# Optimization experiments

Hardware: AMD Instinct MI355X
Metric: run time of the kernel (lower is better)

## Reference

```python
import jax, jax.numpy as jnp
import numpy as np

V = 32          # num_variables
T = 48          # num_time_bins
D = 512         # d_model
H = 8           # num_heads
HD = D // H     # head_dim = 64
OD = 16         # observation_dim
B = 4


def setup_inputs() -> dict:
    key = jax.random.key(0)
    ks = jax.random.split(key, 20)
    s = 0.02
    inp = {
        'h': jax.random.normal(ks[0], (B, T, V, D), jnp.float32),
        'observation_state': jax.random.normal(ks[1], (B, T, V, 2), jnp.float32),
        'Wq': jax.random.normal(ks[2], (D, D), jnp.float32) * s,
        'bq': jnp.zeros((D,), jnp.float32),
        'Wk': jax.random.normal(ks[3], (D, D), jnp.float32) * s,
        'bk': jnp.zeros((D,), jnp.float32),
        'Wv': jax.random.normal(ks[4], (D, D), jnp.float32) * s,
        'bv': jnp.zeros((D,), jnp.float32),
        'Wo': jax.random.normal(ks[5], (D, D), jnp.float32) * s,
        'bo': jnp.zeros((D,), jnp.float32),
        'Woq': jax.random.normal(ks[6], (2, H * OD), jnp.float32) * 0.5,
        'boq': jnp.zeros((H * OD,), jnp.float32),
        'Wok': jax.random.normal(ks[7], (2, H * OD), jnp.float32) * 0.5,
        'bok': jnp.zeros((H * OD,), jnp.float32),
        'variable_bias': jax.random.normal(ks[8], (H, V, V), jnp.float32) * 0.01,
        'relative_time_bias': jax.random.normal(ks[9], (H, 2 * T - 1), jnp.float32) * 0.01,
    }
    return inp


def reference(h, observation_state, Wq, bq, Wk, bk, Wv, bv, Wo, bo,
              Woq, boq, Wok, bok, variable_bias, relative_time_bias):
    N = T * V
    scale = 1.0 / np.sqrt(HD)
    obs_scale = 1.0 / np.sqrt(OD)

    # static index buffers (constants)
    flat_var_ids = jnp.tile(jnp.arange(V), T)                       # [N]
    flat_time_ids = jnp.repeat(jnp.arange(T), V)                    # [N]
    rel_index = flat_time_ids[:, None] - flat_time_ids[None, :] + (T - 1)  # [N,N]

    fh = h.reshape(B, N, D)
    fo = observation_state.reshape(B, N, 2)

    def heads(x, nh, hd):
        return x.reshape(B, N, nh, hd).transpose(0, 2, 1, 3)  # [B,H,N,hd]

    q = heads(fh @ Wq + bq, H, HD)
    k = heads(fh @ Wk + bk, H, HD)
    v = heads(fh @ Wv + bv, H, HD)
    oq = heads(fo @ Woq + boq, H, OD)
    ok = heads(fo @ Wok + bok, H, OD)

    content = jnp.einsum('bhnd,bhmd->bhnm', q, k) * scale
    obs = jnp.einsum('bhnd,bhmd->bhnm', oq, ok) * obs_scale
    var_scores = variable_bias[:, flat_var_ids[:, None], flat_var_ids[None, :]]  # [H,N,N]
    time_scores = relative_time_bias[:, rel_index]                                # [H,N,N]

    scores = content + obs + var_scores[None] + time_scores[None]
    attn = jax.nn.softmax(scores, axis=-1)  # dropout off (inference)
    out = jnp.einsum('bhnm,bhmd->bhnd', attn, v)
    out = out.transpose(0, 2, 1, 3).reshape(B, N, D)
    out = out @ Wo + bo
    return out.reshape(B, T, V, D)
```

## Files before the change

### kernel.cpp

```cpp
#include <hip/hip_runtime.h>
#include <math.h>

typedef __bf16 bf16x8 __attribute__((ext_vector_type(8)));
typedef float f32x4 __attribute__((ext_vector_type(4)));

#define NB 4
#define NT 48
#define NV 32
#define ND 512
#define NH 8
#define NN 1536
#define NBN 6144
#define L2E 1.44269504f

#define GLOAD_LDS(g, l) \
    __builtin_amdgcn_global_load_lds( \
        (const __attribute__((address_space(1))) void*)(g), \
        (__attribute__((address_space(3))) void*)(l), 16, 0, 0)

__global__ __launch_bounds__(256) void prep(
    const float* __restrict__ h, const float* __restrict__ obs,
    const float* __restrict__ Wq, const float* __restrict__ Wk,
    const float* __restrict__ Wv, const float* __restrict__ Wo,
    const float* __restrict__ bq, const float* __restrict__ bk,
    const float* __restrict__ bv,
    const float* __restrict__ Wok, const float* __restrict__ bok,
    __bf16* __restrict__ h_bf, __bf16* __restrict__ WcatT,
    __bf16* __restrict__ WoT, float* __restrict__ biascat,
    __bf16* __restrict__ kx)
{
    __shared__ float ts[64][68];
    const int tid = threadIdx.x;
    const int bx = blockIdx.x;
    if (bx < 1536) {
        int t = bx * 256 + tid;
        const float4* src = (const float4*)h + (size_t)t * 2;
        float4 a = src[0], b = src[1];
        __bf16 r[8] = {(__bf16)a.x, (__bf16)a.y, (__bf16)a.z, (__bf16)a.w,
                       (__bf16)b.x, (__bf16)b.y, (__bf16)b.z, (__bf16)b.w};
        *(uint4*)(h_bf + (size_t)t * 8) = *(uint4*)r;
    } else if (bx < 1792) {
        int bw = bx - 1536;
        const int p = bw >> 6, tile = bw & 63;
        const int k0 = (tile >> 3) * 64, c0 = (tile & 7) * 64;
        const float* W = (p == 0) ? Wq : (p == 1) ? Wk : (p == 2) ? Wv : Wo;
        const float scale = (p == 0) ? 0.125f * L2E : 1.0f;
        #pragma unroll
        for (int i = 0; i < 4; i++) {
            int r = (tid >> 4) + i * 16;
            float4 v = *(const float4*)(W + (size_t)(k0 + r) * 512 + c0 + (tid & 15) * 4);
            *(float4*)&ts[r][(tid & 15) * 4] = v;
        }
        __syncthreads();
        __bf16 tmp[16];
        #pragma unroll
        for (int j = 0; j < 16; j++)
            tmp[j] = (__bf16)(ts[(tid & 3) * 16 + j][tid >> 2] * scale);
        int crow = c0 + (tid >> 2);
        __bf16* dst = (p < 3)
            ? WcatT + ((size_t)(p * 512 + crow)) * 512 + k0 + (tid & 3) * 16
            : WoT   + ((size_t)crow) * 512 + k0 + (tid & 3) * 16;
        *(uint4*)dst = *(uint4*)tmp;
        *(uint4*)(dst + 8) = *(uint4*)(tmp + 8);
        if (p < 3 && k0 == 0 && tid < 64) {
            const float* bb = (p == 0) ? bq : (p == 1) ? bk : bv;
            biascat[p * 512 + c0 + tid] = bb[c0 + tid] * scale;
        }
    } else {
        int t = (bx - 1792) * 256 + tid;
        int row = t >> 1, half = t & 1;
        __bf16* dst = kx + (size_t)row * 96 + 64 + half * 16;
        if (half == 0) {
            int bh = row / NN, n = row - bh * NN;
            int b = bh >> 3, hh = bh & 7;
            size_t bn = (size_t)b * NN + n;
            float o0 = obs[bn * 2], o1 = obs[bn * 2 + 1];
            int f = hh * 16;
            __bf16 tmp[16];
            #pragma unroll
            for (int j = 0; j < 16; j++)
                tmp[j] = (__bf16)(o0 * Wok[f + j] + o1 * Wok[128 + f + j] + bok[f + j]);
            *(uint4*)dst       = *(uint4*)tmp;
            *(uint4*)(dst + 8) = *(uint4*)(tmp + 8);
        } else {
            uint4 z = {0, 0, 0, 0};
            *(uint4*)dst       = z;
            *(uint4*)(dst + 8) = z;
        }
    }
}

template<int TM, bool BF16OUT>
__global__ __launch_bounds__(256) void gemm_mfma(
    const __bf16* __restrict__ A, const __bf16* __restrict__ Bt,
    const float* __restrict__ bias, float* __restrict__ Cf,
    __bf16* __restrict__ qarr, __bf16* __restrict__ kx,
    __bf16* __restrict__ vt)
{
    constexpr int MT = TM / 32;
    __shared__ __align__(16) char smem[34816];
    char* const As0 = smem;
    char* const As1 = smem + TM * 64;
    char* const Bs0 = smem + TM * 128;
    char* const Bs1 = smem + TM * 128 + 8192;
    const int tid = threadIdx.x;
    const int w = tid >> 6, lane = tid & 63;
    const int quad = lane >> 4, l16 = lane & 15;
    const int wm = w >> 1, wn = w & 1;
    const int n0 = blockIdx.x * 128, m0 = blockIdx.y * TM;

    const int sm = tid >> 2;
    const int sk = ((tid & 3) ^ ((sm >> 1) & 3)) * 8;
    const __bf16* aptr = A  + (size_t)(m0 + sm) * 512 + sk;
    const __bf16* bptr = Bt + (size_t)(n0 + sm) * 512 + sk;

    f32x4 zero4 = {0.f, 0.f, 0.f, 0.f};
    f32x4 acc[MT][4];
    #pragma unroll
    for (int i = 0; i < MT; i++)
        #pragma unroll
        for (int j = 0; j < 4; j++) acc[i][j] = zero4;

    auto STAGE = [&](char* dA, char* dB, int kt) {
        GLOAD_LDS(aptr + kt, dA + tid * 16);
        if (TM == 128) GLOAD_LDS(aptr + 64 * 512 + kt, dA + 4096 + tid * 16);
        GLOAD_LDS(bptr + kt, dB + tid * 16);
        GLOAD_LDS(bptr + 64 * 512 + kt, dB + 4096 + tid * 16);
    };
    auto COMPUTE = [&](const char* Asb, const char* Bsb) {
        bf16x8 af[MT], bfr[4];
        #pragma unroll
        for (int mt = 0; mt < MT; mt++) {
            int rr = wm * (TM / 2) + mt * 16 + l16;
            af[mt] = *(const bf16x8*)(Asb + rr * 64 + (quad ^ ((rr >> 1) & 3)) * 16);
        }
        #pragma unroll
        for (int nt = 0; nt < 4; nt++) {
            int rr = wn * 64 + nt * 16 + l16;
            bfr[nt] = *(const bf16x8*)(Bsb + rr * 64 + (quad ^ ((rr >> 1) & 3)) * 16);
        }
        #pragma unroll
        for (int mt = 0; mt < MT; mt++)
            #pragma unroll
            for (int nt = 0; nt < 4; nt++)
                acc[mt][nt] = __builtin_amdgcn_mfma_f32_16x16x32_bf16(
                    af[mt], bfr[nt], acc[mt][nt], 0, 0, 0);
    };

    STAGE(As0, Bs0, 0);
    asm volatile("s_waitcnt vmcnt(0)" ::: "memory");
    __builtin_amdgcn_s_barrier();
    for (int kt = 0; kt < 512; kt += 64) {
        STAGE(As1, Bs1, kt + 32);
        COMPUTE(As0, Bs0);
        asm volatile("s_waitcnt vmcnt(0)" ::: "memory");
        __builtin_amdgcn_s_barrier();
        if (kt + 64 < 512) STAGE(As0, Bs0, kt + 64);
        COMPUTE(As1, Bs1);
        asm volatile("s_waitcnt vmcnt(0)" ::: "memory");
        __builtin_amdgcn_s_barrier();
    }

    __syncthreads();
    if (BF16OUT) {
        if (n0 >= 1024) {
            __bf16* CsT = (__bf16*)smem;
            #pragma unroll
            for (int nt = 0; nt < 4; nt++) {
                int cl = wn * 64 + nt * 16 + l16;
                float bia = bias[n0 + cl];
                #pragma unroll
                for (int mt = 0; mt < MT; mt++) {
                    int rl0 = wm * (TM / 2) + mt * 16 + quad * 4;
                    __bf16 pk[4];
                    #pragma unroll
                    for (int r = 0; r < 4; r++)
                        pk[r] = (__bf16)(acc[mt][nt][r] + bia);
                    *(uint2*)&CsT[cl * 136 + rl0] = *(uint2*)pk;
                }
            }
            __syncthreads();
            int cl = tid >> 1, half = tid & 1;
            int f0 = (n0 + cl) & 511;
            int hh = f0 >> 6, d = f0 & 63;
            int bidx = m0 / NN, nm = m0 - bidx * NN;
            __bf16* dst = vt + ((size_t)(bidx * 8 + hh) * 64 + d) * 1536
                             + nm + half * 64;
            #pragma unroll
            for (int j = 0; j < 8; j++) {
                uint4 v = *(uint4*)&CsT[cl * 136 + half * 64 + j * 8];
                *(uint4*)(dst + j * 8) = v;
            }
        } else {
            __bf16* Cs = (__bf16*)smem;
            #pragma unroll
            for (int mt = 0; mt < MT; mt++)
                #pragma unroll
                for (int nt = 0; nt < 4; nt++) {
                    int cl = wn * 64 + nt * 16 + l16;
                    float bia = bias[n0 + cl];
                    #pragma unroll
                    for (int r = 0; r < 4; r++) {
                        int rl = wm * (TM / 2) + mt * 16 + quad * 4 + r;
                        Cs[rl * 132 + cl] = (__bf16)(acc[mt][nt][r] + bia);
                    }
                }
            __syncthreads();
            int rl = tid >> 1, hb = tid & 1;
            int grow = m0 + rl;
            int col0 = n0 + hb * 64;
            int p = col0 >> 9, f0 = col0 & 511, hh = f0 >> 6;
            int bidx = grow / NN, n = grow - bidx * NN;
            __bf16* dst = (p == 0) ? qarr + (size_t)grow * 512 + f0
                                   : kx + ((size_t)(bidx * 8 + hh) * NN + n) * 96;
            #pragma unroll
            for (int j = 0; j < 8; j++) {
                uint2 lo = *(uint2*)&Cs[rl * 132 + hb * 64 + j * 8];
                uint2 hi = *(uint2*)&Cs[rl * 132 + hb * 64 + j * 8 + 4];
                uint4 v = {lo.x, lo.y, hi.x, hi.y};
                *(uint4*)(dst + j * 8) = v;
            }
        }
    } else {
        float* Csf = (float*)smem;
        #pragma unroll
        for (int mt = 0; mt < MT; mt++)
            #pragma unroll
            for (int nt = 0; nt < 4; nt++) {
                int cl = wn * 64 + nt * 16 + l16;
                float bia = bias[n0 + cl];
                #pragma unroll
                for (int r = 0; r < 4; r++) {
                    int rl = wm * (TM / 2) + mt * 16 + quad * 4 + r;
                    Csf[rl * 132 + cl] = acc[mt][nt][r] + bia;
                }
            }
        __syncthreads();
        int rl = tid >> 2, q4 = tid & 3;
        float* dst = Cf + (size_t)(m0 + rl) * 512 + n0 + q4 * 32;
        #pragma unroll
        for (int j = 0; j < 8; j++) {
            uint4 v = *(uint4*)&Csf[rl * 132 + q4 * 32 + j * 4];
            *(uint4*)(dst + j * 4) = v;
        }
    }
}

__global__ __launch_bounds__(256) void attn_mfma(
    const __bf16* __restrict__ qarr, const __bf16* __restrict__ kx,
    const __bf16* __restrict__ vt, const float* __restrict__ obs,
    const float* __restrict__ Woq, const float* __restrict__ boq,
    const float* __restrict__ varb, const float* __restrict__ rtb,
    __bf16* __restrict__ aout)
{
    __shared__ __align__(16) __bf16 Ks[64][128];
    __shared__ __align__(16) __bf16 Vs0[64][64];
    __shared__ __align__(16) __bf16 Vs1[64][64];
    __shared__ __align__(16) __bf16 Ps[64][64];
    __shared__ float rts[96];

    const int tid = threadIdx.x;
    const int w = tid >> 6, lane = tid & 63;
    const int quad = lane >> 4, l16 = lane & 15;
    const int bh = blockIdx.x, qt = blockIdx.y;
    const int b = bh >> 3, h = bh & 7;
    const int n0 = qt * 64;

    if (tid < 95) rts[tid] = rtb[h * 95 + tid] * L2E;

    const int ck = (tid & 15) ^ ((tid >> 4) & 7);
    const __bf16* kbase = kx + (size_t)bh * NN * 96 + ck * 8;
    const int cv = (tid & 7) ^ ((tid >> 3) & 7);
    const __bf16* vbase = vt + (size_t)bh * 64 * 1536 + cv * 8;

    auto STAGE_K = [&](int m0s) {
        #pragma unroll
        for (int i = 0; i < 4; i++) {
            int row = i * 16 + (tid >> 4);
            GLOAD_LDS(kbase + (size_t)(m0s + row) * 96,
                      (char*)Ks + i * 4096 + tid * 16);
        }
    };
    auto STAGE_V = [&](char* dv, int m0s) {
        #pragma unroll
        for (int i = 0; i < 2; i++) {
            int row = i * 32 + (tid >> 3);
            GLOAD_LDS(vbase + (size_t)row * 1536 + m0s, dv + i * 4096 + tid * 16);
        }
    };

    STAGE_K(0);
    STAGE_V((char*)Vs0, 0);

    const int nl = w * 16 + l16;
    const size_t qrow = (size_t)(b * NN + n0 + nl);
    bf16x8 bq_[3];
    bq_[0] = *(const bf16x8*)(qarr + qrow * 512 + h * 64 + quad * 8);
    bq_[1] = *(const bf16x8*)(qarr + qrow * 512 + h * 64 + 32 + quad * 8);
    {
        uint4 a2u = {0u, 0u, 0u, 0u};
        if (quad < 2) {
            float o0 = obs[qrow * 2], o1 = obs[qrow * 2 + 1];
            int f = h * 16 + quad * 8;
            const float sc = 0.25f * L2E;
            __bf16 tmp[8];
            #pragma unroll
            for (int j = 0; j < 8; j++)
                tmp[j] = (__bf16)(sc * (o0 * Woq[f + j] + o1 * Woq[128 + f + j]
                                        + boq[f + j]));
            a2u = *(uint4*)tmp;
        }
        bq_[2] = *(bf16x8*)&a2u;
    }

    const int rm = (w & 1) * 16 + l16;
    float4 vbA = *(const float4*)(varb + h * 1024 + rm * 32 + quad * 4);
    float4 vbB = *(const float4*)(varb + h * 1024 + rm * 32 + 16 + quad * 4);
    float vA[4] = {vbA.x * L2E, vbA.y * L2E, vbA.z * L2E, vbA.w * L2E};
    float vB[4] = {vbB.x * L2E, vbB.y * L2E, vbB.z * L2E, vbB.w * L2E};
    const int tn = 2 * qt + (w >> 1);

    int wo2[4], ro2[2];
    #pragma unroll
    for (int ct = 0; ct < 4; ct++)
        wo2[ct] = (((ct * 2 + (quad >> 1)) ^ (nl & 7)) * 16) + (quad & 1) * 8;
    #pragma unroll
    for (int ks = 0; ks < 2; ks++)
        ro2[ks] = ((ks * 4 + quad) ^ (nl & 7)) * 16;
    char* psrow = (char*)Ps + nl * 128;

    f32x4 zero4 = {0.f, 0.f, 0.f, 0.f};
    f32x4 o[4];
    f32x4 lpv = zero4;
    #pragma unroll
    for (int i = 0; i < 4; i++) o[i] = zero4;

    asm volatile("s_waitcnt vmcnt(0) lgkmcnt(0)" ::: "memory");
    __builtin_amdgcn_s_barrier();

    const char* Vcur = (const char*)Vs0;
    char* Vnxt = (char*)Vs1;

    for (int mt = 0; mt < 24; mt++) {
        f32x4 sc[4];
        __builtin_amdgcn_s_setprio(1);
        #pragma unroll
        for (int ct = 0; ct < 4; ct++) {
            f32x4 d = zero4;
            int row = ct * 16 + l16;
            #pragma unroll
            for (int ks = 0; ks < 3; ks++) {
                bf16x8 kf = *(const bf16x8*)((const char*)Ks + row * 256
                                + (((ks * 4 + quad) ^ (row & 7)) * 16));
                d = __builtin_amdgcn_mfma_f32_16x16x32_bf16(kf, bq_[ks], d, 0, 0, 0);
            }
            sc[ct] = d;
        }
        __builtin_amdgcn_s_setprio(0);

        asm volatile("s_waitcnt lgkmcnt(0)" ::: "memory");
        __builtin_amdgcn_s_barrier();

        if (mt + 1 < 24) {
            STAGE_K((mt + 1) * 64);
            STAGE_V(Vnxt, (mt + 1) * 64);
        }

        float tb0 = rts[tn - 2 * mt + 47];
        float tb1 = rts[tn - 2 * mt + 46];
        #pragma unroll
        for (int ct = 0; ct < 4; ct++) {
            float tb = (ct & 2) ? tb1 : tb0;
            const float* vv = (ct & 1) ? vB : vA;
            __bf16 pk[4];
            #pragma unroll
            for (int r = 0; r < 4; r++) {
                float p = exp2f(sc[ct][r] + tb + vv[r]);
                lpv[r] += p;
                pk[r] = (__bf16)p;
            }
            *(uint2*)(psrow + wo2[ct]) = *(uint2*)pk;
        }

        __builtin_amdgcn_s_setprio(1);
        #pragma unroll
        for (int ks = 0; ks < 2; ks++) {
            bf16x8 pf = *(const bf16x8*)(psrow + ro2[ks]);
            #pragma unroll
            for (int dt = 0; dt < 4; dt++) {
                int rw = dt * 16 + l16;
                bf16x8 vf = *(const bf16x8*)(Vcur + rw * 128
                                + (((ks * 4 + quad) ^ (rw & 7)) * 16));
                o[dt] = __builtin_amdgcn_mfma_f32_16x16x32_bf16(vf, pf, o[dt], 0, 0, 0);
            }
        }
        __builtin_amdgcn_s_setprio(0);

        asm volatile("s_waitcnt vmcnt(0)" ::: "memory");
        __builtin_amdgcn_s_barrier();

        const char* t = Vcur; Vcur = (const char*)Vnxt; Vnxt = (char*)t;
    }

    float lp = (lpv[0] + lpv[1]) + (lpv[2] + lpv[3]);
    lp += __shfl_xor(lp, 16);
    lp += __shfl_xor(lp, 32);
    float inv = 1.0f / lp;
    size_t abase = ((size_t)b * NN + n0 + nl) * 512 + h * 64 + quad * 4;
    #pragma unroll
    for (int dt = 0; dt < 4; dt++) {
        __bf16 ov[4];
        #pragma unroll
        for (int r = 0; r < 4; r++) ov[r] = (__bf16)(o[dt][r] * inv);
        *(uint2*)(aout + abase + dt * 16) = *(uint2*)ov;
    }
}

extern "C" void kernel_launch(void* const* d_in, const int* in_sizes, int n_in,
                              void* d_out, int out_size, void* d_ws, size_t ws_size,
                              hipStream_t stream)
{
    const float* h_   = (const float*)d_in[0];
    const float* obs  = (const float*)d_in[1];
    const float* Wq   = (const float*)d_in[2];
    const float* bq   = (const float*)d_in[3];
    const float* Wk   = (const float*)d_in[4];
    const float* bk   = (const float*)d_in[5];
    const float* Wv   = (const float*)d_in[6];
    const float* bv   = (const float*)d_in[7];
    const float* Wo   = (const float*)d_in[8];
    const float* bo   = (const float*)d_in[9];
    const float* Woq  = (const float*)d_in[10];
    const float* boq  = (const float*)d_in[11];
    const float* Wok  = (const float*)d_in[12];
    const float* bok  = (const float*)d_in[13];
    const float* varb = (const float*)d_in[14];
    const float* rtb  = (const float*)d_in[15];
    float* out = (float*)d_out;

    char* ws = (char*)d_ws;
    __bf16* h_bf    = (__bf16*)ws;                 ws += (size_t)NBN * 512 * 2;
    __bf16* qarr    = (__bf16*)ws;                 ws += (size_t)NBN * 512 * 2;
    __bf16* vt      = (__bf16*)ws;                 ws += (size_t)NBN * 512 * 2;
    __bf16* kx      = (__bf16*)ws;                 ws += ((size_t)32 * NN * 96 + 64) * 2;
    __bf16* attnout = (__bf16*)ws;                 ws += (size_t)NBN * 512 * 2;
    __bf16* WcatT   = (__bf16*)ws;                 ws += (size_t)1536 * 512 * 2;
    __bf16* WoT     = (__bf16*)ws;                 ws += (size_t)512 * 512 * 2;
    float*  biascat = (float*)ws;                  ws += 1536 * 4;

    prep<<<dim3(2176), dim3(256), 0, stream>>>(
        h_, obs, Wq, Wk, Wv, Wo, bq, bk, bv, Wok, bok,
        h_bf, WcatT, WoT, biascat, kx);
    gemm_mfma<128, true><<<dim3(12, 48), dim3(256), 0, stream>>>(
        h_bf, WcatT, biascat, nullptr, qarr, kx, vt);
    attn_mfma<<<dim3(32, 24), dim3(256), 0, stream>>>(qarr, kx, vt, obs, Woq, boq,
                                                      varb, rtb, attnout);
    gemm_mfma<64, false><<<dim3(4, 96), dim3(256), 0, stream>>>(
        attnout, WoT, bo, out, nullptr, nullptr, nullptr);
}
```

Before: 184.2 us.

## Store V in MFMA fragment order and load it directly into registers

The QKV GEMM epilogue now writes V^T in a per-64-key-tile layout that matches the MFMA B-fragment order, one 16-byte chunk per lane. The attention kernel drops the double-buffered V staging through LDS and loads each lane's V fragments straight from global memory at the top of every key tile. This removes LDS traffic and the V share of the staging, at the cost of exposed global-load latency inside the loop (only the K compute hides it), and every wave in a block re-reads the same V data from cache.

```diff
diff --git a/kernel.cpp b/kernel.cpp
--- a/kernel.cpp
+++ b/kernel.cpp
@@ -183,13 +183,16 @@
             int cl = tid >> 1, half = tid & 1;
             int f0 = (n0 + cl) & 511;
             int hh = f0 >> 6, d = f0 & 63;
+            int dt = d >> 4, l16v = d & 15;
             int bidx = m0 / NN, nm = m0 - bidx * NN;
-            __bf16* dst = vt + ((size_t)(bidx * 8 + hh) * 64 + d) * 1536
-                             + nm + half * 64;
+            int bh = bidx * 8 + hh;
+            int mtv = (nm >> 6) + half;
+            __bf16* dstb = vt + ((size_t)(bh * 24 + mtv)) * 4096 + l16v * 8;
             #pragma unroll
             for (int j = 0; j < 8; j++) {
                 uint4 v = *(uint4*)&CsT[cl * 136 + half * 64 + j * 8];
-                *(uint4*)(dst + j * 8) = v;
+                int frag = dt * 2 + (j >> 2), qd = j & 3;
+                *(uint4*)(dstb + (frag * 4 + qd) * 128) = v;
             }
         } else {
             __bf16* Cs = (__bf16*)smem;
@@ -254,8 +257,6 @@
     __bf16* __restrict__ aout)
 {
     __shared__ __align__(16) __bf16 Ks[64][128];
-    __shared__ __align__(16) __bf16 Vs0[64][64];
-    __shared__ __align__(16) __bf16 Vs1[64][64];
     __shared__ __align__(16) __bf16 Ps[64][64];
     __shared__ float rts[96];
 
@@ -270,8 +271,7 @@
 
     const int ck = (tid & 15) ^ ((tid >> 4) & 7);
     const __bf16* kbase = kx + (size_t)bh * NN * 96 + ck * 8;
-    const int cv = (tid & 7) ^ ((tid >> 3) & 7);
-    const __bf16* vbase = vt + (size_t)bh * 64 * 1536 + cv * 8;
+    const __bf16* vtile = vt + (size_t)bh * 24 * 4096 + lane * 8;
 
     auto STAGE_K = [&](int m0s) {
         #pragma unroll
@@ -281,16 +281,8 @@
                       (char*)Ks + i * 4096 + tid * 16);
         }
     };
-    auto STAGE_V = [&](char* dv, int m0s) {
-        #pragma unroll
-        for (int i = 0; i < 2; i++) {
-            int row = i * 32 + (tid >> 3);
-            GLOAD_LDS(vbase + (size_t)row * 1536 + m0s, dv + i * 4096 + tid * 16);
-        }
-    };
 
     STAGE_K(0);
-    STAGE_V((char*)Vs0, 0);
 
     const int nl = w * 16 + l16;
     const size_t qrow = (size_t)(b * NN + n0 + nl);
@@ -338,10 +330,15 @@
     asm volatile("s_waitcnt vmcnt(0) lgkmcnt(0)" ::: "memory");
     __builtin_amdgcn_s_barrier();
 
-    const char* Vcur = (const char*)Vs0;
-    char* Vnxt = (char*)Vs1;
-
     for (int mt = 0; mt < 24; mt++) {
+        const __bf16* vtm = vtile + (size_t)mt * 4096;
+        bf16x8 vfr[4][2];
+        #pragma unroll
+        for (int dt = 0; dt < 4; dt++)
+            #pragma unroll
+            for (int ks = 0; ks < 2; ks++)
+                vfr[dt][ks] = *(const bf16x8*)(vtm + (dt * 2 + ks) * 512);
+
         f32x4 sc[4];
         __builtin_amdgcn_s_setprio(1);
         #pragma unroll
@@ -361,10 +358,7 @@
         asm volatile("s_waitcnt lgkmcnt(0)" ::: "memory");
         __builtin_amdgcn_s_barrier();
 
-        if (mt + 1 < 24) {
-            STAGE_K((mt + 1) * 64);
-            STAGE_V(Vnxt, (mt + 1) * 64);
-        }
+        if (mt + 1 < 24) STAGE_K((mt + 1) * 64);
 
         float tb0 = rts[tn - 2 * mt + 47];
         float tb1 = rts[tn - 2 * mt + 46];
@@ -387,19 +381,14 @@
         for (int ks = 0; ks < 2; ks++) {
             bf16x8 pf = *(const bf16x8*)(psrow + ro2[ks]);
             #pragma unroll
-            for (int dt = 0; dt < 4; dt++) {
-                int rw = dt * 16 + l16;
-                bf16x8 vf = *(const bf16x8*)(Vcur + rw * 128
-                                + (((ks * 4 + quad) ^ (rw & 7)) * 16));
-                o[dt] = __builtin_amdgcn_mfma_f32_16x16x32_bf16(vf, pf, o[dt], 0, 0, 0);
-            }
+            for (int dt = 0; dt < 4; dt++)
+                o[dt] = __builtin_amdgcn_mfma_f32_16x16x32_bf16(
+                    vfr[dt][ks], pf, o[dt], 0, 0, 0);
         }
         __builtin_amdgcn_s_setprio(0);
 
         asm volatile("s_waitcnt vmcnt(0)" ::: "memory");
         __builtin_amdgcn_s_barrier();
-
-        const char* t = Vcur; Vcur = (const char*)Vnxt; Vnxt = (char*)t;
     }
 
     float lp = (lpv[0] + lpv[1]) + (lpv[2] + lpv[3]);
@@ -445,7 +434,7 @@
     __bf16* kx      = (__bf16*)ws;                 ws += ((size_t)32 * NN * 96 + 64) * 2;
     __bf16* attnout = (__bf16*)ws;                 ws += (size_t)NBN * 512 * 2;
     __bf16* WcatT   = (__bf16*)ws;                 ws += (size_t)1536 * 512 * 2;
-    __bf16* WoT     = (__bf16*)ws;                 ws += (size_t)512 * 512 * 2;
+    __bf16* WoT    = (__bf16*)ws;                  ws += (size_t)512 * 512 * 2;
     float*  biascat = (float*)ws;                  ws += 1536 * 4;
 
     prep<<<dim3(2176), dim3(256), 0, stream>>>(
```

New measurement: 181.7 us. About the same (-1.3%).
